# Performance work log

Hardware: AMD Instinct MI355X
Metric: run time of the kernel (lower is better)

The kernel has to match this reference:

```python
import jax, jax.numpy as jnp
import numpy as np

BS, N, D_IN, HID, D_OUT = 16, 256, 128, 128, 128


def setup_inputs() -> dict:
    key = jax.random.key(0)
    ks = jax.random.split(key, 10)
    s = 0.02
    return {
        "x": jax.random.normal(ks[0], (BS, N, D_IN), dtype=jnp.float32),
        "adj": jax.random.randint(ks[1], (BS, N, N), 0, 2, dtype=jnp.int32),
        "W_fc": jax.random.normal(ks[2], (D_IN, HID), dtype=jnp.float32) * s,
        "b_fc": jnp.zeros((HID,), dtype=jnp.float32),
        "W_a1": jax.random.normal(ks[3], (2 * HID, HID), dtype=jnp.float32) * s,
        "b_a1": jnp.zeros((HID,), dtype=jnp.float32),
        "w_a2": jax.random.normal(ks[4], (HID,), dtype=jnp.float32) * s,
        "b_a2": jnp.zeros((), dtype=jnp.float32),
        "W_out": jax.random.normal(ks[5], (HID, D_OUT), dtype=jnp.float32) * s,
        "b_out": jnp.zeros((D_OUT,), dtype=jnp.float32),
    }


def reference(x, adj, W_fc, b_fc, W_a1, b_a1, w_a2, b_a2, W_out, b_out):
    # h = fc(x): (bs, n, hid)
    h = jnp.einsum("bnd,dh->bnh", x, W_fc) + b_fc
    # attn first layer on concat([h_i, h_j]) decomposes into two half-projections
    # (same math as Linear(2*hid, hid) on the concatenated pair features).
    a_i = jnp.einsum("bnh,hk->bnk", h, W_a1[:HID])  # contribution of h_i
    a_j = jnp.einsum("bnh,hk->bnk", h, W_a1[HID:])  # contribution of h_j
    pre = a_i[:, :, None, :] + a_j[:, None, :, :] + b_a1  # (bs, n, n, hid)
    e = jnp.einsum("bijk,k->bij", jax.nn.relu(pre), w_a2) + b_a2  # (bs, n, n)
    e = jnp.where(adj == 0, jnp.float32(-1e9), e)
    attn = jax.nn.softmax(e, axis=-1)
    h_prime = jnp.einsum("bij,bjh->bih", attn, h)
    out = jnp.einsum("bih,ho->bio", h_prime, W_out) + b_out
    return out
```

## Files before the change

### kernel.cpp

```cpp
#include <hip/hip_runtime.h>

#define BS  16
#define NN  256
#define HID 128

__device__ __forceinline__ int xcd_swz(int bid) {
    return (bid & 7) * 64 + (bid >> 3);
}

__global__ __launch_bounds__(512, 4) void gat_k1(
    const float* __restrict__ x, const float* __restrict__ W_fc,
    const float* __restrict__ b_fc, const float* __restrict__ W_a1,
    const float* __restrict__ b_a1, const float* __restrict__ W_out,
    float* __restrict__ aiT, float* __restrict__ ajT, float* __restrict__ g)
{
    __shared__ __align__(16) float xs[8][HID];
    __shared__ __align__(16) float hs[8][HID];
    __shared__ __align__(16) float red[4][3][8][HID];

    const int tid = threadIdx.x;
    const int k   = tid & 127;
    const int q   = tid >> 7;
    const int swz = xcd_swz(blockIdx.x);
    const int r0  = swz * 8;
    const int b   = r0 >> 8;
    const int n0  = r0 & 255;

    for (int t = tid; t < 8 * HID; t += 512)
        xs[t >> 7][t & 127] = x[r0 * HID + t];
    __syncthreads();

    {
        float acc[8] = {0,0,0,0,0,0,0,0};
        const int dq = 32 * q;
        #pragma unroll 2
        for (int d = 0; d < 32; d += 4) {
            float w[4];
            #pragma unroll
            for (int t = 0; t < 4; ++t) w[t] = W_fc[(dq + d + t) * HID + k];
            #pragma unroll
            for (int r = 0; r < 8; ++r) {
                const float4 xv = *(const float4*)&xs[r][dq + d];
                acc[r] += xv.x * w[0] + xv.y * w[1] + xv.z * w[2] + xv.w * w[3];
            }
        }
        #pragma unroll
        for (int r = 0; r < 8; ++r) red[q][0][r][k] = acc[r];
    }
    __syncthreads();

    {
        const float bf = b_fc[k];
        #pragma unroll
        for (int r2 = 0; r2 < 2; ++r2) {
            const int r = 2 * q + r2;
            hs[r][k] = (red[0][0][r][k] + red[1][0][r][k])
                     + (red[2][0][r][k] + red[3][0][r][k]) + bf;
        }
    }
    __syncthreads();

    {
        float ai_a[8] = {0,0,0,0,0,0,0,0};
        float aj_a[8] = {0,0,0,0,0,0,0,0};
        float g_a[8]  = {0,0,0,0,0,0,0,0};
        const int dq = 32 * q;
        #pragma unroll 2
        for (int d = 0; d < 32; d += 4) {
            float wi[4], wj[4], wo[4];
            #pragma unroll
            for (int t = 0; t < 4; ++t) {
                wi[t] = W_a1[(dq + d + t) * HID + k];
                wj[t] = W_a1[(HID + dq + d + t) * HID + k];
                wo[t] = W_out[(dq + d + t) * HID + k];
            }
            #pragma unroll
            for (int r = 0; r < 8; ++r) {
                const float4 hv = *(const float4*)&hs[r][dq + d];
                ai_a[r] += hv.x * wi[0] + hv.y * wi[1] + hv.z * wi[2] + hv.w * wi[3];
                aj_a[r] += hv.x * wj[0] + hv.y * wj[1] + hv.z * wj[2] + hv.w * wj[3];
                g_a[r]  += hv.x * wo[0] + hv.y * wo[1] + hv.z * wo[2] + hv.w * wo[3];
            }
        }
        #pragma unroll
        for (int r = 0; r < 8; ++r) {
            red[q][0][r][k] = ai_a[r];
            red[q][1][r][k] = aj_a[r];
            red[q][2][r][k] = g_a[r];
        }
    }
    __syncthreads();

    {
        const int is_aj = q >> 1;
        const int rb4   = (q & 1) * 4;
        const float bias = is_aj ? 0.f : b_a1[k];
        float4 v;
        v.x = (red[0][is_aj][rb4 + 0][k] + red[1][is_aj][rb4 + 0][k])
            + (red[2][is_aj][rb4 + 0][k] + red[3][is_aj][rb4 + 0][k]) + bias;
        v.y = (red[0][is_aj][rb4 + 1][k] + red[1][is_aj][rb4 + 1][k])
            + (red[2][is_aj][rb4 + 1][k] + red[3][is_aj][rb4 + 1][k]) + bias;
        v.z = (red[0][is_aj][rb4 + 2][k] + red[1][is_aj][rb4 + 2][k])
            + (red[2][is_aj][rb4 + 2][k] + red[3][is_aj][rb4 + 2][k]) + bias;
        v.w = (red[0][is_aj][rb4 + 3][k] + red[1][is_aj][rb4 + 3][k])
            + (red[2][is_aj][rb4 + 3][k] + red[3][is_aj][rb4 + 3][k]) + bias;
        float* dst = (is_aj ? ajT : aiT) + (b * HID + k) * NN + n0 + rb4;
        *(float4*)dst = v;

        #pragma unroll
        for (int r2 = 0; r2 < 2; ++r2) {
            const int r = 2 * q + r2;
            g[(r0 + r) * HID + k] = (red[0][2][r][k] + red[1][2][r][k])
                                  + (red[2][2][r][k] + red[3][2][r][k]);
        }
    }
}

__global__ __launch_bounds__(512, 4) void gat_k2(
    const float* __restrict__ aiT, const float* __restrict__ ajT,
    const float* __restrict__ g,  const int* __restrict__ adj,
    const float* __restrict__ w_a2, const float* __restrict__ b_a2,
    const float* __restrict__ b_out, float* __restrict__ out)
{
    __shared__ __align__(16) float aiw[HID][8];
    __shared__ __align__(16) float w2s[HID];
    __shared__ __align__(16) float buf[2][8][NN];
    __shared__ __align__(16) float ep[8][NN];

    const int tid = threadIdx.x;
    const int swz = xcd_swz(blockIdx.x);
    const int b   = swz >> 5;
    const int i0  = (swz & 31) * 8;
    const int wv  = tid >> 6, lane = tid & 63;

    for (int t = tid; t < HID * 8; t += 512) {
        const int kk = t >> 3, r = t & 7;
        aiw[kk][r] = aiT[(b * HID + kk) * NN + i0 + r];
    }
    if (tid < HID) w2s[tid] = w_a2[tid];

    const int4 am = *(const int4*)(adj + (b * NN + i0 + wv) * NN + 4 * lane);
    __syncthreads();

    const int kh = wv >> 2, rp = wv & 3;
    {
        const float* ajp = ajT + (b * HID + kh * 64) * NN + 4 * lane;
        float4 acc0 = {0,0,0,0}, acc1 = {0,0,0,0}, saw = {0,0,0,0};
        const int kb = kh * 64;
        #pragma unroll 8
        for (int t = 0; t < 64; ++t) {
            const float4 a4 = *(const float4*)(ajp + t * NN);
            const float2 f2 = *(const float2*)&aiw[kb + t][2 * rp];
            const float wk  = w2s[kb + t];
            saw.x  = __builtin_fmaf(a4.x, wk, saw.x);
            saw.y  = __builtin_fmaf(a4.y, wk, saw.y);
            saw.z  = __builtin_fmaf(a4.z, wk, saw.z);
            saw.w  = __builtin_fmaf(a4.w, wk, saw.w);
            acc0.x = __builtin_fmaf(fmaxf(f2.x, -a4.x), wk, acc0.x);
            acc0.y = __builtin_fmaf(fmaxf(f2.x, -a4.y), wk, acc0.y);
            acc0.z = __builtin_fmaf(fmaxf(f2.x, -a4.z), wk, acc0.z);
            acc0.w = __builtin_fmaf(fmaxf(f2.x, -a4.w), wk, acc0.w);
            acc1.x = __builtin_fmaf(fmaxf(f2.y, -a4.x), wk, acc1.x);
            acc1.y = __builtin_fmaf(fmaxf(f2.y, -a4.y), wk, acc1.y);
            acc1.z = __builtin_fmaf(fmaxf(f2.y, -a4.z), wk, acc1.z);
            acc1.w = __builtin_fmaf(fmaxf(f2.y, -a4.w), wk, acc1.w);
        }
        const float4 e0 = {acc0.x + saw.x, acc0.y + saw.y,
                           acc0.z + saw.z, acc0.w + saw.w};
        const float4 e1 = {acc1.x + saw.x, acc1.y + saw.y,
                           acc1.z + saw.z, acc1.w + saw.w};
        *(float4*)&buf[kh][2 * rp + 0][4 * lane] = e0;
        *(float4*)&buf[kh][2 * rp + 1][4 * lane] = e1;
    }
    __syncthreads();

    {
        const float ba2 = b_a2[0];
        const float4 u = *(const float4*)&buf[0][wv][4 * lane];
        const float4 v = *(const float4*)&buf[1][wv][4 * lane];
        const float e0 = am.x ? u.x + v.x + ba2 : -1e9f;
        const float e1 = am.y ? u.y + v.y + ba2 : -1e9f;
        const float e2 = am.z ? u.z + v.z + ba2 : -1e9f;
        const float e3 = am.w ? u.w + v.w + ba2 : -1e9f;
        float m = fmaxf(fmaxf(e0, e1), fmaxf(e2, e3));
        #pragma unroll
        for (int off = 32; off; off >>= 1) m = fmaxf(m, __shfl_xor(m, off));
        const float p0 = __expf(e0 - m), p1 = __expf(e1 - m);
        const float p2 = __expf(e2 - m), p3 = __expf(e3 - m);
        float s = (p0 + p1) + (p2 + p3);
        #pragma unroll
        for (int off = 32; off; off >>= 1) s += __shfl_xor(s, off);
        const float inv = 1.f / s;
        const float4 pv = {p0 * inv, p1 * inv, p2 * inv, p3 * inv};
        *(float4*)&ep[wv][4 * lane] = pv;
    }
    __syncthreads();

    float* red = &buf[0][0][0];
    const int k = tid & 127, qh = tid >> 7;
    {
        float o[8] = {0,0,0,0,0,0,0,0};
        const float* gb = g + (b * NN + qh * 64) * HID + k;
        const int jb = qh * 64;
        #pragma unroll 2
        for (int jq = 0; jq < 64; jq += 4) {
            const float g0 = gb[(jq + 0) * HID];
            const float g1 = gb[(jq + 1) * HID];
            const float g2 = gb[(jq + 2) * HID];
            const float g3 = gb[(jq + 3) * HID];
            #pragma unroll
            for (int r = 0; r < 8; ++r) {
                const float4 pv = *(const float4*)&ep[r][jb + jq];
                o[r] += pv.x * g0 + pv.y * g1 + pv.z * g2 + pv.w * g3;
            }
        }
        #pragma unroll
        for (int r = 0; r < 8; ++r) red[(qh * 8 + r) * HID + k] = o[r];
    }
    __syncthreads();

    {
        const float bo = b_out[k];
        #pragma unroll
        for (int r2 = 0; r2 < 2; ++r2) {
            const int r = 2 * qh + r2;
            out[(b * NN + i0 + r) * HID + k] =
                (red[(0 + r) * HID + k]  + red[(8 + r) * HID + k]) +
                (red[(16 + r) * HID + k] + red[(24 + r) * HID + k]) + bo;
        }
    }
}

extern "C" void kernel_launch(void* const* d_in, const int* in_sizes, int n_in,
                              void* d_out, int out_size, void* d_ws, size_t ws_size,
                              hipStream_t stream) {
    const float* x     = (const float*)d_in[0];
    const int*   adj   = (const int*)  d_in[1];
    const float* W_fc  = (const float*)d_in[2];
    const float* b_fc  = (const float*)d_in[3];
    const float* W_a1  = (const float*)d_in[4];
    const float* b_a1  = (const float*)d_in[5];
    const float* w_a2  = (const float*)d_in[6];
    const float* b_a2  = (const float*)d_in[7];
    const float* W_out = (const float*)d_in[8];
    const float* b_out = (const float*)d_in[9];
    float* out = (float*)d_out;

    float* ws  = (float*)d_ws;
    float* aiT = ws;
    float* ajT = ws + BS * NN * HID;
    float* g   = ws + 2 * BS * NN * HID;

    gat_k1<<<BS * NN / 8, 512, 0, stream>>>(x, W_fc, b_fc, W_a1, b_a1, W_out,
                                            aiT, ajT, g);
    gat_k2<<<BS * (NN / 8), 512, 0, stream>>>(aiT, ajT, g, adj, w_a2, b_a2,
                                              b_out, out);
}
```

Measured before the change: 40.86 us.

## Rebalance gat_k2 work split: 4 rows per wave in scores, 8-way j split in aggregation

The score phase now gives each wave 4 query rows over 32 hidden channels instead of 2 rows over 64. Each loaded ajT float4 is reused across more rows, and the aiT tile is loaded as float4 pairs. The aggregation phase splits j across all 8 waves, with each lane handling 2 output columns through float2 loads, and the final reduction sums 8 partials. This cuts redundant global loads of ajT and g per block, at the cost of more registers, a larger shared buffer (4x8x256) and a longer final reduction.

Result: faster. 36.03 us, median of 2 (-11.8%).

```diff
diff --git a/kernel.cpp b/kernel.cpp
--- a/kernel.cpp
+++ b/kernel.cpp
@@ -122,10 +122,10 @@
     const float* __restrict__ w_a2, const float* __restrict__ b_a2,
     const float* __restrict__ b_out, float* __restrict__ out)
 {
-    __shared__ __align__(16) float aiw[HID][8];
-    __shared__ __align__(16) float w2s[HID];
-    __shared__ __align__(16) float buf[2][8][NN];
-    __shared__ __align__(16) float ep[8][NN];
+    __shared__ __align__(16) float4 aiwp[HID][2];
+    __shared__ __align__(16) float  w2s[HID];
+    __shared__ __align__(16) float  buf4[4][8][NN];
+    __shared__ __align__(16) float  ep[8][NN];
 
     const int tid = threadIdx.x;
     const int swz = xcd_swz(blockIdx.x);
@@ -133,55 +133,75 @@
     const int i0  = (swz & 31) * 8;
     const int wv  = tid >> 6, lane = tid & 63;
 
-    for (int t = tid; t < HID * 8; t += 512) {
-        const int kk = t >> 3, r = t & 7;
-        aiw[kk][r] = aiT[(b * HID + kk) * NN + i0 + r];
-    }
-    if (tid < HID) w2s[tid] = w_a2[tid];
-
+    if (tid < 256) {
+        const int kk = tid >> 1, rh = tid & 1;
+        aiwp[kk][rh] = *(const float4*)&aiT[(b * HID + kk) * NN + i0 + 4 * rh];
+    } else if (tid < 384) {
+        w2s[tid - 256] = w_a2[tid - 256];
+    }
     const int4 am = *(const int4*)(adj + (b * NN + i0 + wv) * NN + 4 * lane);
     __syncthreads();
 
-    const int kh = wv >> 2, rp = wv & 3;
-    {
-        const float* ajp = ajT + (b * HID + kh * 64) * NN + 4 * lane;
-        float4 acc0 = {0,0,0,0}, acc1 = {0,0,0,0}, saw = {0,0,0,0};
-        const int kb = kh * 64;
+    {
+        const int kh = wv >> 1, rh = wv & 1;
+        const float* ajp = ajT + (b * HID + kh * 32) * NN + 4 * lane;
+        float4 acc0 = {0,0,0,0}, acc1 = {0,0,0,0};
+        float4 acc2 = {0,0,0,0}, acc3 = {0,0,0,0};
+        float4 saw  = {0,0,0,0};
+        const int kb = kh * 32;
         #pragma unroll 8
-        for (int t = 0; t < 64; ++t) {
+        for (int t = 0; t < 32; ++t) {
             const float4 a4 = *(const float4*)(ajp + t * NN);
-            const float2 f2 = *(const float2*)&aiw[kb + t][2 * rp];
+            const float4 aw = aiwp[kb + t][rh];
             const float wk  = w2s[kb + t];
             saw.x  = __builtin_fmaf(a4.x, wk, saw.x);
             saw.y  = __builtin_fmaf(a4.y, wk, saw.y);
             saw.z  = __builtin_fmaf(a4.z, wk, saw.z);
             saw.w  = __builtin_fmaf(a4.w, wk, saw.w);
-            acc0.x = __builtin_fmaf(fmaxf(f2.x, -a4.x), wk, acc0.x);
-            acc0.y = __builtin_fmaf(fmaxf(f2.x, -a4.y), wk, acc0.y);
-            acc0.z = __builtin_fmaf(fmaxf(f2.x, -a4.z), wk, acc0.z);
-            acc0.w = __builtin_fmaf(fmaxf(f2.x, -a4.w), wk, acc0.w);
-            acc1.x = __builtin_fmaf(fmaxf(f2.y, -a4.x), wk, acc1.x);
-            acc1.y = __builtin_fmaf(fmaxf(f2.y, -a4.y), wk, acc1.y);
-            acc1.z = __builtin_fmaf(fmaxf(f2.y, -a4.z), wk, acc1.z);
-            acc1.w = __builtin_fmaf(fmaxf(f2.y, -a4.w), wk, acc1.w);
-        }
-        const float4 e0 = {acc0.x + saw.x, acc0.y + saw.y,
-                           acc0.z + saw.z, acc0.w + saw.w};
-        const float4 e1 = {acc1.x + saw.x, acc1.y + saw.y,
-                           acc1.z + saw.z, acc1.w + saw.w};
-        *(float4*)&buf[kh][2 * rp + 0][4 * lane] = e0;
-        *(float4*)&buf[kh][2 * rp + 1][4 * lane] = e1;
+            acc0.x = __builtin_fmaf(fmaxf(aw.x, -a4.x), wk, acc0.x);
+            acc0.y = __builtin_fmaf(fmaxf(aw.x, -a4.y), wk, acc0.y);
+            acc0.z = __builtin_fmaf(fmaxf(aw.x, -a4.z), wk, acc0.z);
+            acc0.w = __builtin_fmaf(fmaxf(aw.x, -a4.w), wk, acc0.w);
+            acc1.x = __builtin_fmaf(fmaxf(aw.y, -a4.x), wk, acc1.x);
+            acc1.y = __builtin_fmaf(fmaxf(aw.y, -a4.y), wk, acc1.y);
+            acc1.z = __builtin_fmaf(fmaxf(aw.y, -a4.z), wk, acc1.z);
+            acc1.w = __builtin_fmaf(fmaxf(aw.y, -a4.w), wk, acc1.w);
+            acc2.x = __builtin_fmaf(fmaxf(aw.z, -a4.x), wk, acc2.x);
+            acc2.y = __builtin_fmaf(fmaxf(aw.z, -a4.y), wk, acc2.y);
+            acc2.z = __builtin_fmaf(fmaxf(aw.z, -a4.z), wk, acc2.z);
+            acc2.w = __builtin_fmaf(fmaxf(aw.z, -a4.w), wk, acc2.w);
+            acc3.x = __builtin_fmaf(fmaxf(aw.w, -a4.x), wk, acc3.x);
+            acc3.y = __builtin_fmaf(fmaxf(aw.w, -a4.y), wk, acc3.y);
+            acc3.z = __builtin_fmaf(fmaxf(aw.w, -a4.z), wk, acc3.z);
+            acc3.w = __builtin_fmaf(fmaxf(aw.w, -a4.w), wk, acc3.w);
+        }
+        const int rb = 4 * rh;
+        float4 e;
+        e.x = acc0.x + saw.x; e.y = acc0.y + saw.y;
+        e.z = acc0.z + saw.z; e.w = acc0.w + saw.w;
+        *(float4*)&buf4[kh][rb + 0][4 * lane] = e;
+        e.x = acc1.x + saw.x; e.y = acc1.y + saw.y;
+        e.z = acc1.z + saw.z; e.w = acc1.w + saw.w;
+        *(float4*)&buf4[kh][rb + 1][4 * lane] = e;
+        e.x = acc2.x + saw.x; e.y = acc2.y + saw.y;
+        e.z = acc2.z + saw.z; e.w = acc2.w + saw.w;
+        *(float4*)&buf4[kh][rb + 2][4 * lane] = e;
+        e.x = acc3.x + saw.x; e.y = acc3.y + saw.y;
+        e.z = acc3.z + saw.z; e.w = acc3.w + saw.w;
+        *(float4*)&buf4[kh][rb + 3][4 * lane] = e;
     }
     __syncthreads();
 
     {
         const float ba2 = b_a2[0];
-        const float4 u = *(const float4*)&buf[0][wv][4 * lane];
-        const float4 v = *(const float4*)&buf[1][wv][4 * lane];
-        const float e0 = am.x ? u.x + v.x + ba2 : -1e9f;
-        const float e1 = am.y ? u.y + v.y + ba2 : -1e9f;
-        const float e2 = am.z ? u.z + v.z + ba2 : -1e9f;
-        const float e3 = am.w ? u.w + v.w + ba2 : -1e9f;
+        const float4 s0 = *(const float4*)&buf4[0][wv][4 * lane];
+        const float4 s1 = *(const float4*)&buf4[1][wv][4 * lane];
+        const float4 s2 = *(const float4*)&buf4[2][wv][4 * lane];
+        const float4 s3 = *(const float4*)&buf4[3][wv][4 * lane];
+        const float e0 = am.x ? (s0.x + s1.x) + (s2.x + s3.x) + ba2 : -1e9f;
+        const float e1 = am.y ? (s0.y + s1.y) + (s2.y + s3.y) + ba2 : -1e9f;
+        const float e2 = am.z ? (s0.z + s1.z) + (s2.z + s3.z) + ba2 : -1e9f;
+        const float e3 = am.w ? (s0.w + s1.w) + (s2.w + s3.w) + ba2 : -1e9f;
         float m = fmaxf(fmaxf(e0, e1), fmaxf(e2, e3));
         #pragma unroll
         for (int off = 32; off; off >>= 1) m = fmaxf(m, __shfl_xor(m, off));
@@ -196,37 +216,43 @@
     }
     __syncthreads();
 
-    float* red = &buf[0][0][0];
-    const int k = tid & 127, qh = tid >> 7;
-    {
-        float o[8] = {0,0,0,0,0,0,0,0};
-        const float* gb = g + (b * NN + qh * 64) * HID + k;
-        const int jb = qh * 64;
+    float* red = &buf4[0][0][0];
+    {
+        float2 o[8];
+        #pragma unroll
+        for (int r = 0; r < 8; ++r) { o[r].x = 0.f; o[r].y = 0.f; }
+        const int jb = 32 * wv;
+        const float* gb = g + (b * NN + jb) * HID + 2 * lane;
         #pragma unroll 2
-        for (int jq = 0; jq < 64; jq += 4) {
-            const float g0 = gb[(jq + 0) * HID];
-            const float g1 = gb[(jq + 1) * HID];
-            const float g2 = gb[(jq + 2) * HID];
-            const float g3 = gb[(jq + 3) * HID];
+        for (int jq = 0; jq < 32; jq += 4) {
+            const float2 g0 = *(const float2*)(gb + (jq + 0) * HID);
+            const float2 g1 = *(const float2*)(gb + (jq + 1) * HID);
+            const float2 g2 = *(const float2*)(gb + (jq + 2) * HID);
+            const float2 g3 = *(const float2*)(gb + (jq + 3) * HID);
             #pragma unroll
             for (int r = 0; r < 8; ++r) {
                 const float4 pv = *(const float4*)&ep[r][jb + jq];
-                o[r] += pv.x * g0 + pv.y * g1 + pv.z * g2 + pv.w * g3;
-            }
-        }
-        #pragma unroll
-        for (int r = 0; r < 8; ++r) red[(qh * 8 + r) * HID + k] = o[r];
-    }
-    __syncthreads();
-
-    {
+                o[r].x += pv.x * g0.x + pv.y * g1.x + pv.z * g2.x + pv.w * g3.x;
+                o[r].y += pv.x * g0.y + pv.y * g1.y + pv.z * g2.y + pv.w * g3.y;
+            }
+        }
+        #pragma unroll
+        for (int r = 0; r < 8; ++r)
+            *(float2*)&red[(wv * 8 + r) * HID + 2 * lane] = o[r];
+    }
+    __syncthreads();
+
+    {
+        const int k = tid & 127, q = tid >> 7;
         const float bo = b_out[k];
         #pragma unroll
         for (int r2 = 0; r2 < 2; ++r2) {
-            const int r = 2 * qh + r2;
-            out[(b * NN + i0 + r) * HID + k] =
-                (red[(0 + r) * HID + k]  + red[(8 + r) * HID + k]) +
-                (red[(16 + r) * HID + k] + red[(24 + r) * HID + k]) + bo;
+            const int r = 2 * q + r2;
+            float s = 0.f;
+            #pragma unroll
+            for (int oct = 0; oct < 8; ++oct)
+                s += red[(oct * 8 + r) * HID + k];
+            out[(b * NN + i0 + r) * HID + k] = s + bo;
         }
     }
 }
```
